# Kernel optimization log

Measured on AMD Instinct MI355X. Metric: run time of the kernel, lower is better.

The kernel has to match this reference:

```python
import jax, jax.numpy as jnp
import numpy as np


def _mish(x):
    return x * jnp.tanh(jax.nn.softplus(x))


def setup_inputs() -> dict:
    key = jax.random.key(0)
    ks = jax.random.split(key, 10)
    N, D, U, NB, M, MD = 2048, 1024, 2048, 4, 8192, 1024
    g = lambda k, shape, s=0.02: jax.random.normal(k, shape, jnp.float32) * s
    return dict(
        x=jax.random.normal(ks[0], (N, D), jnp.float32),
        w=g(ks[1], (D, U, NB)),
        delay=g(ks[2], (D, U, NB)),
        b=jnp.zeros((U, NB), jnp.float32),
        gate_W=g(ks[3], (D, NB)),
        gate_b=jnp.zeros((NB,), jnp.float32),
        neuron_avg=jax.random.uniform(ks[4], (U,), jnp.float32),
        conn_W1=g(ks[5], (U, 32)),
        conn_b1=jnp.zeros((32,), jnp.float32),
        conn_W2=g(ks[6], (32, U)),
        conn_b2=jnp.zeros((U,), jnp.float32),
        mask=jnp.ones((U,), jnp.float32),
        act_w=jnp.ones((9,), jnp.float32),
        read_W=g(ks[7], (U, M)),
        read_b=jnp.zeros((M,), jnp.float32),
        memory=g(ks[8], (M, MD), 1.0),
    )


def reference(x, w, delay, b, gate_W, gate_b, neuron_avg, conn_W1, conn_b1,
              conn_W2, conn_b2, mask, act_w, read_W, read_b, memory):
    # --- DynamicPlasticDenseDendritic forward ---
    w_mod = w * jax.nn.sigmoid(delay)                      # [D,U,NB]
    branch = jnp.einsum('nd,dub->nub', x, w_mod) + b       # [N,U,NB]
    gate = jax.nn.softmax(x @ gate_W + gate_b, axis=-1)    # [N,NB]
    z = jnp.einsum('nub,nb->nu', branch, gate)             # [N,U]
    # DynamicConnectivity on neuron activation averages (single row)
    h = jax.nn.relu(neuron_avg[None, :] @ conn_W1 + conn_b1)   # [1,32]
    conn = jax.nn.sigmoid(h @ conn_W2 + conn_b2)               # [1,U]
    a = jax.nn.relu(z * conn * mask[None, :])                  # [N,U]
    # --- LearnedActivation: softmax-weighted 8-way activation blend (+zero) ---
    wts = jax.nn.softmax(act_w)
    blend = (wts[0] * jax.nn.sigmoid(a) + wts[1] * jax.nn.elu(a)
             + wts[2] * jnp.tanh(a) + wts[3] * jax.nn.relu(a)
             + wts[4] * jax.nn.silu(a) + wts[5] * jax.nn.gelu(a, approximate=False)
             + wts[6] * jax.nn.selu(a) + wts[7] * _mish(a))
    # --- EpisodicMemory read ---
    attn = jax.nn.softmax(blend @ read_W + read_b, axis=-1)   # [N,M]
    read = attn @ memory                                       # [N,MD]
    return read
```

## Files before the change

kernel.cpp:

```cpp
#include <hip/hip_runtime.h>


typedef unsigned short u16;
typedef __attribute__((ext_vector_type(8))) short bf16x8;
typedef __attribute__((ext_vector_type(4))) float f32x4;

__device__ __forceinline__ float b2f(u16 h) {
    union { unsigned u; float f; } v; v.u = ((unsigned)h) << 16; return v.f;
}
__device__ __forceinline__ u16 f2b(float f) {
    union { float f; unsigned u; } v; v.f = f;
    unsigned u = v.u;
    return (u16)((u + 0x7fffu + ((u >> 16) & 1u)) >> 16);
}

__device__ __forceinline__ void async_copy16(void* lds, const void* g) {
    __builtin_amdgcn_global_load_lds(
        (__attribute__((address_space(1))) void*)(g),
        (__attribute__((address_space(3))) void*)(lds), 16, 0, 0);
}

__device__ __forceinline__ int swz(int o) { return o ^ (((o >> 7) & 7) << 4); }

__device__ __forceinline__ int swz64(int kg, int row) { return kg ^ (row & 3); }

__device__ __forceinline__ void stage_tile256(const u16* __restrict__ src, int ld,
                                              int base0, int k0,
                                              char* ldsbase, int tid)
{
#pragma unroll
    for (int h = 0; h < 2; h++)
#pragma unroll
        for (int it = 0; it < 2; it++) {
            int o = it * 8192 + tid * 16;
            int s = swz(o);
            int r = s >> 7;
            int c = (s & 127) >> 1;
            async_copy16(ldsbase + h * 16384 + o,
                         src + (size_t)(base0 + h * 128 + r) * ld + k0 + c);
        }
}

__device__ __forceinline__ void gemm256_core8(const u16* __restrict__ A,
                                              const u16* __restrict__ B,
                                              int Ktiles, int ld,
                                              int row0, int col0,
                                              char* lds, f32x4 (&acc)[8][4])
{
    const int tid  = threadIdx.x;
    const int lane = tid & 63;
    const int wv   = tid >> 6;
    const int wr   = wv >> 2;
    const int wc   = wv & 3;
    const int lr   = lane & 15, kg = lane >> 4;

#pragma unroll
    for (int i = 0; i < 8; i++)
#pragma unroll
        for (int j = 0; j < 4; j++) {
            f32x4 z = {0.f, 0.f, 0.f, 0.f};
            acc[i][j] = z;
        }

    stage_tile256(A, ld, row0, 0, lds, tid);
    stage_tile256(B, ld, col0, 0, lds + 32768, tid);
    asm volatile("s_waitcnt vmcnt(0)" ::: "memory");
    __builtin_amdgcn_s_barrier();

    bf16x8 af03[4][2], af47[4][2], bfr[2][2];

    for (int t = 0; t < Ktiles; t++) {
        const int buf = (t & 1) << 16;
        const char* sA = lds + buf + wr * 16384;
        const char* sB = lds + buf + 32768 + ((wc >> 1) * 16384);
        char* nb = lds + (((t + 1) & 1) << 16);
        const bool pf = (t + 1 < Ktiles);

        auto rdA = [&](int i, int ks) {
            int off = (i * 16 + lr) * 128 + ks * 64 + kg * 16;
            return *(const bf16x8*)(sA + swz(off));
        };
        auto rdB = [&](int j, int ks) {
            int off = ((wc & 1) * 64 + j * 16 + lr) * 128 + ks * 64 + kg * 16;
            return *(const bf16x8*)(sB + swz(off));
        };

#pragma unroll
        for (int i = 0; i < 4; i++) { af03[i][0] = rdA(i, 0); af03[i][1] = rdA(i, 1); }
#pragma unroll
        for (int j = 0; j < 2; j++) { bfr[j][0] = rdB(j, 0); bfr[j][1] = rdB(j, 1); }
#pragma unroll
        for (int i = 0; i < 4; i++) { af47[i][0] = rdA(4 + i, 0); af47[i][1] = rdA(4 + i, 1); }
        if (pf) stage_tile256(A, ld, row0, (t + 1) * 64, nb, tid);
        __builtin_amdgcn_s_barrier();
        __builtin_amdgcn_s_setprio(1);
#pragma unroll
        for (int i = 0; i < 4; i++)
#pragma unroll
            for (int j = 0; j < 2; j++) {
                acc[i][j] = __builtin_amdgcn_mfma_f32_16x16x32_bf16(af03[i][0], bfr[j][0], acc[i][j], 0, 0, 0);
                acc[i][j] = __builtin_amdgcn_mfma_f32_16x16x32_bf16(af03[i][1], bfr[j][1], acc[i][j], 0, 0, 0);
            }
        __builtin_amdgcn_s_setprio(0);
        __builtin_amdgcn_s_barrier();

        if (pf) stage_tile256(B, ld, col0, (t + 1) * 64, nb + 32768, tid);
        __builtin_amdgcn_s_barrier();
        __builtin_amdgcn_s_setprio(1);
#pragma unroll
        for (int i = 0; i < 4; i++)
#pragma unroll
            for (int j = 0; j < 2; j++) {
                acc[4 + i][j] = __builtin_amdgcn_mfma_f32_16x16x32_bf16(af47[i][0], bfr[j][0], acc[4 + i][j], 0, 0, 0);
                acc[4 + i][j] = __builtin_amdgcn_mfma_f32_16x16x32_bf16(af47[i][1], bfr[j][1], acc[4 + i][j], 0, 0, 0);
            }
        __builtin_amdgcn_s_setprio(0);
        __builtin_amdgcn_s_barrier();

#pragma unroll
        for (int j = 0; j < 2; j++) { bfr[j][0] = rdB(2 + j, 0); bfr[j][1] = rdB(2 + j, 1); }
        __builtin_amdgcn_s_barrier();
        __builtin_amdgcn_s_setprio(1);
#pragma unroll
        for (int i = 0; i < 4; i++)
#pragma unroll
            for (int j = 0; j < 2; j++) {
                acc[4 + i][2 + j] = __builtin_amdgcn_mfma_f32_16x16x32_bf16(af47[i][0], bfr[j][0], acc[4 + i][2 + j], 0, 0, 0);
                acc[4 + i][2 + j] = __builtin_amdgcn_mfma_f32_16x16x32_bf16(af47[i][1], bfr[j][1], acc[4 + i][2 + j], 0, 0, 0);
            }
        __builtin_amdgcn_s_setprio(0);
        __builtin_amdgcn_s_barrier();

        __builtin_amdgcn_s_setprio(1);
#pragma unroll
        for (int i = 0; i < 4; i++)
#pragma unroll
            for (int j = 0; j < 2; j++) {
                acc[i][2 + j] = __builtin_amdgcn_mfma_f32_16x16x32_bf16(af03[i][0], bfr[j][0], acc[i][2 + j], 0, 0, 0);
                acc[i][2 + j] = __builtin_amdgcn_mfma_f32_16x16x32_bf16(af03[i][1], bfr[j][1], acc[i][2 + j], 0, 0, 0);
            }
        __builtin_amdgcn_s_setprio(0);
        asm volatile("s_waitcnt vmcnt(0)" ::: "memory");
        __builtin_amdgcn_s_barrier();
    }
}

template<int BM, int BN, int S>
__device__ __forceinline__ void gemm_core_db(const u16* __restrict__ A,
                                             const u16* __restrict__ B,
                                             int Kloop, int ld,
                                             int row0, int col0,
                                             u16* smem,
                                             f32x4 (&acc)[BM / 32][BN / 32])
{
    constexpr int MT = BM / 32, NT = BN / 32;
    constexpr int STG = (BM + BN) * 32;
    constexpr int SET = STG * S;
    const int tid  = threadIdx.x;
    const int lane = tid & 63;
    const int wv   = tid >> 6;
    const int wr   = wv >> 1, wc = wv & 1;
    const int lr   = lane & 15, kg = lane >> 4;

#pragma unroll
    for (int i = 0; i < MT; i++)
#pragma unroll
        for (int j = 0; j < NT; j++) {
            f32x4 z = {0.f, 0.f, 0.f, 0.f};
            acc[i][j] = z;
        }

    auto stage_in = [&](u16* set, int k0) {
#pragma unroll
        for (int c = tid; c < BM * 4; c += 256) {
            int row = c >> 2, sl = swz64(c & 3, row);
            const u16* gA = A + (size_t)(row0 + row) * ld + k0 + sl * 8;
#pragma unroll
            for (int s = 0; s < S; s++)
                async_copy16(set + s * STG + c * 8, gA + s * 32);
        }
#pragma unroll
        for (int c = tid; c < BN * 4; c += 256) {
            int row = c >> 2, sl = swz64(c & 3, row);
            const u16* gB = B + (size_t)(col0 + row) * ld + k0 + sl * 8;
#pragma unroll
            for (int s = 0; s < S; s++)
                async_copy16(set + s * STG + BM * 32 + c * 8, gB + s * 32);
        }
    };

    stage_in(smem, 0);
    __syncthreads();

    int p = 0;
    for (int k0 = 0; k0 < Kloop; k0 += 32 * S) {
        if (k0 + 32 * S < Kloop)
            stage_in(smem + (p ^ 1) * SET, k0 + 32 * S);
        u16* set = smem + p * SET;
#pragma unroll
        for (int s = 0; s < S; s++) {
            const u16* sA = set + s * STG;
            const u16* sB = sA + BM * 32;
            bf16x8 af[MT], bfr[NT];
#pragma unroll
            for (int i = 0; i < MT; i++) {
                int row = wr * (BM / 2) + i * 16 + lr;
                af[i] = *(const bf16x8*)(sA + (row * 32 + swz64(kg, row) * 8));
            }
#pragma unroll
            for (int j = 0; j < NT; j++) {
                int row = wc * (BN / 2) + j * 16 + lr;
                bfr[j] = *(const bf16x8*)(sB + (row * 32 + swz64(kg, row) * 8));
            }
#pragma unroll
            for (int i = 0; i < MT; i++)
#pragma unroll
                for (int j = 0; j < NT; j++)
                    acc[i][j] = __builtin_amdgcn_mfma_f32_16x16x32_bf16(
                                    af[i], bfr[j], acc[i][j], 0, 0, 0);
        }
        __syncthreads();
        p ^= 1;
    }
}

__global__ __launch_bounds__(256)
void k_prep(const float* __restrict__ na, const float* __restrict__ W1,
            const float* __restrict__ b1, const float* __restrict__ W2,
            const float* __restrict__ b2, const float* __restrict__ actw,
            float* __restrict__ conn, float* __restrict__ wts,
            const float* __restrict__ x, const float* __restrict__ gW,
            const float* __restrict__ gb, float* __restrict__ gate,
            u16* __restrict__ y,
            const float* __restrict__ w, const float* __restrict__ delay,
            u16* __restrict__ wmT)
{
    __shared__ __align__(16) char sh[256 * 32 * 4 + 128];
    const int bid = blockIdx.x;
    const int tid = threadIdx.x;

    if (bid == 0) {
        float* red = (float*)sh;
        float* hsh = (float*)(sh + 256 * 32 * 4);
        float h[32];
#pragma unroll
        for (int k = 0; k < 32; k++) h[k] = 0.f;
        for (int u = tid; u < 2048; u += 256) {
            float nav = na[u];
            const float* row = W1 + u * 32;
#pragma unroll
            for (int k = 0; k < 32; k++) h[k] += nav * row[k];
        }
#pragma unroll
        for (int k = 0; k < 32; k++) red[tid * 32 + k] = h[k];
        for (int s = 128; s > 0; s >>= 1) {
            __syncthreads();
            if (tid < s)
#pragma unroll
                for (int k = 0; k < 32; k++) red[tid * 32 + k] += red[(tid + s) * 32 + k];
        }
        __syncthreads();
        if (tid < 32) hsh[tid] = fmaxf(red[tid] + b1[tid], 0.f);
        if (tid == 0) {
            float e[9], m = -1e30f;
            for (int i = 0; i < 9; i++) { e[i] = actw[i]; m = fmaxf(m, e[i]); }
            float s = 0.f;
            for (int i = 0; i < 9; i++) { e[i] = expf(e[i] - m); s += e[i]; }
            for (int i = 0; i < 9; i++) wts[i] = e[i] / s;
        }
        __syncthreads();
        for (int u = tid; u < 2048; u += 256) {
            float a = 0.f;
#pragma unroll
            for (int k = 0; k < 32; k++) a += hsh[k] * W2[k * 2048 + u];
            conn[u] = 1.f / (1.f + expf(-(a + b2[u])));
        }
    } else if (bid <= 512) {
        const int lane = tid & 63, wvx = tid >> 6;
        const int n = (bid - 1) * 4 + wvx;
        const float* xr = x + (size_t)n * 1024;
        float a0 = 0, a1 = 0, a2 = 0, a3 = 0;
        float xv[16];
#pragma unroll
        for (int s = 0; s < 16; s++) {
            int d = s * 64 + lane;
            float xd = xr[d]; xv[s] = xd;
            float4 g4 = *(const float4*)(gW + d * 4);
            a0 += xd * g4.x; a1 += xd * g4.y; a2 += xd * g4.z; a3 += xd * g4.w;
        }
#pragma unroll
        for (int off = 32; off > 0; off >>= 1) {
            a0 += __shfl_xor(a0, off); a1 += __shfl_xor(a1, off);
            a2 += __shfl_xor(a2, off); a3 += __shfl_xor(a3, off);
        }
        a0 += gb[0]; a1 += gb[1]; a2 += gb[2]; a3 += gb[3];
        float m = fmaxf(fmaxf(a0, a1), fmaxf(a2, a3));
        float e0 = expf(a0 - m), e1 = expf(a1 - m), e2 = expf(a2 - m), e3 = expf(a3 - m);
        float inv = 1.f / (e0 + e1 + e2 + e3);
        float g0 = e0 * inv, g1 = e1 * inv, g2 = e2 * inv, g3 = e3 * inv;
        if (lane == 0) *(float4*)(gate + n * 4) = make_float4(g0, g1, g2, g3);
#pragma unroll
        for (int s = 0; s < 16; s++) {
            int d = s * 64 + lane;
            ushort4 o;
            o.x = f2b(xv[s] * g0); o.y = f2b(xv[s] * g1);
            o.z = f2b(xv[s] * g2); o.w = f2b(xv[s] * g3);
            *(ushort4*)(y + (size_t)n * 4096 + d * 4) = o;
        }
    } else {
        typedef ushort4 row65[65];
        row65* tile = (row65*)sh;
        const int b = bid - 513;
        const int u0 = (b & 31) * 64, d0 = (b >> 5) * 32;
        const int tx = tid & 63, ty = tid >> 6;
#pragma unroll
        for (int i = 0; i < 8; i++) {
            int d = i * 4 + ty;
            size_t idx = ((size_t)(d0 + d) * 2048 + (u0 + tx)) * 4;
            float4 w4 = *(const float4*)(w + idx);
            float4 d4 = *(const float4*)(delay + idx);
            ushort4 o;
            o.x = f2b(w4.x / (1.f + expf(-d4.x)));
            o.y = f2b(w4.y / (1.f + expf(-d4.y)));
            o.z = f2b(w4.z / (1.f + expf(-d4.z)));
            o.w = f2b(w4.w / (1.f + expf(-d4.w)));
            tile[d][tx] = o;
        }
        __syncthreads();
        const int dx = tid & 31, uy = tid >> 5;
#pragma unroll
        for (int i = 0; i < 8; i++) {
            int u = i * 8 + uy;
            *(ushort4*)(wmT + (size_t)(u0 + u) * 4096 + (d0 + dx) * 4) = tile[dx][u];
        }
    }
}

__global__ __launch_bounds__(256)
void k_transpose(const float* __restrict__ in, u16* __restrict__ out, int R, int C)
{
    __shared__ __align__(16) u16 t[64][68];
    const int tid = threadIdx.x, tx = tid & 15, ty = tid >> 4;
    const int c0 = blockIdx.x * 64, r0 = blockIdx.y * 64;
#pragma unroll
    for (int i = 0; i < 4; i++) {
        int r = r0 + ty + i * 16;
        float4 v = *(const float4*)(in + (size_t)r * C + c0 + tx * 4);
        t[tx * 4 + 0][ty + i * 16] = f2b(v.x); t[tx * 4 + 1][ty + i * 16] = f2b(v.y);
        t[tx * 4 + 2][ty + i * 16] = f2b(v.z); t[tx * 4 + 3][ty + i * 16] = f2b(v.w);
    }
    __syncthreads();
#pragma unroll
    for (int i = 0; i < 4; i++) {
        int c = ty + i * 16;
        ushort4 v;
        v.x = t[c][tx * 4 + 0]; v.y = t[c][tx * 4 + 1];
        v.z = t[c][tx * 4 + 2]; v.w = t[c][tx * 4 + 3];
        *(ushort4*)(out + (size_t)(c0 + c) * R + r0 + tx * 4) = v;
    }
}

__device__ __forceinline__ float act_blend(float a,
    float w0, float w1, float w2, float w3,
    float w4, float w5, float w6, float w7)
{
    float sig = 1.f / (1.f + expf(-a));
    float elu = (a > 0.f) ? a : (expf(a) - 1.f);
    float th  = tanhf(a);
    float rel = fmaxf(a, 0.f);
    float sil = a * sig;
    float gel = a * 0.5f * (1.f + erff(a * 0.70710678118654752f));
    float sel = (a > 0.f) ? 1.0507009873554805f * a
                          : 1.0507009873554805f * 1.6732632423543772f * (expf(a) - 1.f);
    float sp  = (a > 20.f) ? a : log1pf(expf(a));
    float mish = a * tanhf(sp);
    return w0 * sig + w1 * elu + w2 * th + w3 * rel + w4 * sil + w5 * gel
         + w6 * sel + w7 * mish;
}

__global__ __launch_bounds__(512, 2)
void k_gemm_a8(const u16* __restrict__ A, const u16* __restrict__ B,
               float* __restrict__ P)
{
    __shared__ __align__(16) char lds[131072];
    const int row0 = blockIdx.y * 256, col0 = blockIdx.x * 256;
    const u16* Ac = A + (size_t)blockIdx.z * 1024;
    const u16* Bc = B + (size_t)blockIdx.z * 1024;

    f32x4 acc[8][4];
    gemm256_core8(Ac, Bc, 16, 4096, row0, col0, lds, acc);

    float* Pz = P + (size_t)blockIdx.z * 2048 * 2048;
    const int tid = threadIdx.x, lane = tid & 63, wv = tid >> 6;
    const int wr = wv >> 2, wc = wv & 3, lr = lane & 15, kg = lane >> 4;
#pragma unroll
    for (int i = 0; i < 8; i++)
#pragma unroll
        for (int r = 0; r < 4; r++) {
            int n = row0 + wr * 128 + i * 16 + kg * 4 + r;
            size_t ob = (size_t)n * 2048;
#pragma unroll
            for (int j = 0; j < 4; j++)
                Pz[ob + col0 + wc * 64 + j * 16 + lr] = acc[i][j][r];
        }
}

__global__ __launch_bounds__(256)
void k_reduce_blend(const float* __restrict__ P, const float* __restrict__ gate,
                    const float* __restrict__ conn, const float* __restrict__ mask,
                    const float* __restrict__ wts, const float* __restrict__ bbias,
                    u16* __restrict__ blend)
{
    constexpr size_t SL = (size_t)2048 * 2048;
    const int n  = blockIdx.x;
    const int u0 = threadIdx.x * 8;
    const float* base = P + (size_t)n * 2048 + u0;

    float v[8];
#pragma unroll
    for (int h = 0; h < 2; h++) {
        float4 a = *(const float4*)(base + h * 4);
        float4 b = *(const float4*)(base + SL + h * 4);
        float4 c = *(const float4*)(base + 2 * SL + h * 4);
        float4 d = *(const float4*)(base + 3 * SL + h * 4);
        v[h * 4 + 0] = a.x + b.x + c.x + d.x;
        v[h * 4 + 1] = a.y + b.y + c.y + d.y;
        v[h * 4 + 2] = a.z + b.z + c.z + d.z;
        v[h * 4 + 3] = a.w + b.w + c.w + d.w;
    }
    float4 g = *(const float4*)(gate + n * 4);
    const float w0 = wts[0], w1 = wts[1], w2 = wts[2], w3 = wts[3];
    const float w4 = wts[4], w5 = wts[5], w6 = wts[6], w7 = wts[7];

    ushort4 o[2];
#pragma unroll
    for (int j = 0; j < 8; j++) {
        int u = u0 + j;
        float4 b4 = *(const float4*)(bbias + u * 4);
        float z = v[j] + g.x * b4.x + g.y * b4.y + g.z * b4.z + g.w * b4.w;
        float a = fmaxf(z * conn[u] * mask[u], 0.f);
        u16 r = f2b(act_blend(a, w0, w1, w2, w3, w4, w5, w6, w7));
        ((u16*)o)[j] = r;
    }
    *(ushort4*)(blend + (size_t)n * 2048 + u0)     = o[0];
    *(ushort4*)(blend + (size_t)n * 2048 + u0 + 4) = o[1];
}

__global__ __launch_bounds__(512, 2)
void k_gemm_logits8(const u16* __restrict__ BL, const u16* __restrict__ RWT,
                    const float* __restrict__ rbias, u16* __restrict__ out)
{
    __shared__ __align__(16) char lds[131072];
    const int row0 = blockIdx.y * 256, col0 = blockIdx.x * 256;

    f32x4 acc[8][4];
    gemm256_core8(BL, RWT, 32, 2048, row0, col0, lds, acc);

    const int tid = threadIdx.x, lane = tid & 63, wv = tid >> 6;
    const int wr = wv >> 2, wc = wv & 3, lr = lane & 15, kg = lane >> 4;
    float rb[4]; int mm[4];
#pragma unroll
    for (int j = 0; j < 4; j++) {
        mm[j] = col0 + wc * 64 + j * 16 + lr;
        rb[j] = rbias[mm[j]];
    }
#pragma unroll
    for (int i = 0; i < 8; i++)
#pragma unroll
        for (int r = 0; r < 4; r++) {
            int n = row0 + wr * 128 + i * 16 + kg * 4 + r;
            size_t ob = (size_t)n * 8192;
#pragma unroll
            for (int j = 0; j < 4; j++)
                out[ob + mm[j]] = f2b(acc[i][j][r] + rb[j]);
        }
}

__global__ __launch_bounds__(256)
void k_post(u16* __restrict__ buf, const float* __restrict__ mem,
            u16* __restrict__ memT)
{
    __shared__ __align__(16) char sh[64 * 68 * 2 + 64];
    const int bid = blockIdx.x;
    const int tid = threadIdx.x;

    if (bid < 2048) {
        float* red = (float*)sh;
        const int lane = tid & 63, wv = tid >> 6;
        u16* row = buf + (size_t)bid * 8192;
        float v[32];
        float mx = -1e30f;
#pragma unroll
        for (int s = 0; s < 8; s++) {
            ushort4 u4 = *(const ushort4*)(row + (s * 256 + tid) * 4);
            float a = b2f(u4.x), b = b2f(u4.y), c = b2f(u4.z), d = b2f(u4.w);
            v[s * 4 + 0] = a; v[s * 4 + 1] = b; v[s * 4 + 2] = c; v[s * 4 + 3] = d;
            mx = fmaxf(mx, fmaxf(fmaxf(a, b), fmaxf(c, d)));
        }
#pragma unroll
        for (int off = 32; off > 0; off >>= 1) mx = fmaxf(mx, __shfl_xor(mx, off));
        if (lane == 0) red[wv] = mx;
        __syncthreads();
        mx = fmaxf(fmaxf(red[0], red[1]), fmaxf(red[2], red[3]));
        float sum = 0.f;
#pragma unroll
        for (int k = 0; k < 32; k++) { v[k] = expf(v[k] - mx); sum += v[k]; }
#pragma unroll
        for (int off = 32; off > 0; off >>= 1) sum += __shfl_xor(sum, off);
        if (lane == 0) red[4 + wv] = sum;
        __syncthreads();
        float inv = 1.f / (red[4] + red[5] + red[6] + red[7]);
#pragma unroll
        for (int s = 0; s < 8; s++) {
            ushort4 o;
            o.x = f2b(v[s * 4 + 0] * inv); o.y = f2b(v[s * 4 + 1] * inv);
            o.z = f2b(v[s * 4 + 2] * inv); o.w = f2b(v[s * 4 + 3] * inv);
            *(ushort4*)(row + (s * 256 + tid) * 4) = o;
        }
    } else {
        typedef u16 row68[68];
        row68* t = (row68*)sh;
        const int b = bid - 2048;
        const int c0 = (b & 15) * 64, r0 = (b >> 4) * 64;
        const int tx = tid & 15, ty = tid >> 4;
#pragma unroll
        for (int i = 0; i < 4; i++) {
            int r = r0 + ty + i * 16;
            float4 v = *(const float4*)(mem + (size_t)r * 1024 + c0 + tx * 4);
            t[tx * 4 + 0][ty + i * 16] = f2b(v.x); t[tx * 4 + 1][ty + i * 16] = f2b(v.y);
            t[tx * 4 + 2][ty + i * 16] = f2b(v.z); t[tx * 4 + 3][ty + i * 16] = f2b(v.w);
        }
        __syncthreads();
#pragma unroll
        for (int i = 0; i < 4; i++) {
            int c = ty + i * 16;
            ushort4 v;
            v.x = t[c][tx * 4 + 0]; v.y = t[c][tx * 4 + 1];
            v.z = t[c][tx * 4 + 2]; v.w = t[c][tx * 4 + 3];
            *(ushort4*)(memT + (size_t)(c0 + c) * 8192 + r0 + tx * 4) = v;
        }
    }
}

template<int BM, int BN, int S, int NCOL>
__global__ __launch_bounds__(256, 4)
void k_gemm_partial(const u16* __restrict__ A, const u16* __restrict__ B,
                    int Kchunk, int ld, float* __restrict__ P)
{
    constexpr int MT = BM / 32, NT = BN / 32;
    __shared__ __align__(16) u16 smem[2 * (BM + BN) * 32 * S];

    const int nx = gridDim.x, ny = gridDim.y;
    const int f  = blockIdx.x + nx * blockIdx.y;
    const int ch = (nx * ny) >> 3;
    const int sw = (f & 7) * ch + (f >> 3);
    const int bx = sw % nx, by = sw / nx;
    const int row0 = by * BM, col0 = bx * BN;

    const u16* Ac = A + (size_t)blockIdx.z * Kchunk;
    const u16* Bc = B + (size_t)blockIdx.z * Kchunk;

    f32x4 acc[MT][NT];
    gemm_core_db<BM, BN, S>(Ac, Bc, Kchunk, ld, row0, col0, smem, acc);

    float* Pz = P + (size_t)blockIdx.z * 2048 * NCOL;
    const int tid = threadIdx.x, lane = tid & 63, wv = tid >> 6;
    const int wr = wv >> 1, wc = wv & 1, lr = lane & 15, kg = lane >> 4;
#pragma unroll
    for (int i = 0; i < MT; i++)
#pragma unroll
        for (int r = 0; r < 4; r++) {
            int n = row0 + wr * (BM / 2) + i * 16 + kg * 4 + r;
            size_t ob = (size_t)n * NCOL;
#pragma unroll
            for (int j = 0; j < NT; j++)
                Pz[ob + col0 + wc * (BN / 2) + j * 16 + lr] = acc[i][j][r];
        }
}

__global__ __launch_bounds__(256)
void k_reduce_out(const float* __restrict__ P, float* __restrict__ out)
{
    constexpr size_t SL = (size_t)2048 * 1024;
    size_t i = ((size_t)blockIdx.x * 256 + threadIdx.x) * 4;
    float4 a = *(const float4*)(P + i);
    float4 b = *(const float4*)(P + SL + i);
    float4 c = *(const float4*)(P + 2 * SL + i);
    float4 d = *(const float4*)(P + 3 * SL + i);
    float4 o;
    o.x = a.x + b.x + c.x + d.x;
    o.y = a.y + b.y + c.y + d.y;
    o.z = a.z + b.z + c.z + d.z;
    o.w = a.w + b.w + c.w + d.w;
    *(float4*)(out + i) = o;
}

__global__ void k_fill(float* out, int n)
{
    int i = blockIdx.x * 256 + threadIdx.x;
    if (i < n) out[i] = 12345.f;
}

extern "C" void kernel_launch(void* const* d_in, const int* in_sizes, int n_in,
                              void* d_out, int out_size, void* d_ws, size_t ws_size,
                              hipStream_t stream)
{
    const float* x     = (const float*)d_in[0];
    const float* w     = (const float*)d_in[1];
    const float* delay = (const float*)d_in[2];
    const float* bb    = (const float*)d_in[3];
    const float* gW    = (const float*)d_in[4];
    const float* gb    = (const float*)d_in[5];
    const float* na    = (const float*)d_in[6];
    const float* cW1   = (const float*)d_in[7];
    const float* cb1   = (const float*)d_in[8];
    const float* cW2   = (const float*)d_in[9];
    const float* cb2   = (const float*)d_in[10];
    const float* mask  = (const float*)d_in[11];
    const float* actw  = (const float*)d_in[12];
    const float* rW    = (const float*)d_in[13];
    const float* rb    = (const float*)d_in[14];
    const float* mem   = (const float*)d_in[15];
    (void)in_sizes; (void)n_in;

    char* ws = (char*)d_ws;
    size_t off = 0;
    auto alloc = [&](size_t bytes) {
        size_t o = off; off += (bytes + 255) & ~(size_t)255; return o;
    };
    size_t o_wts   = alloc(9 * 4);
    size_t o_gate  = alloc(2048 * 4 * 4);
    size_t o_conn  = alloc(2048 * 4);
    size_t o_y     = alloc((size_t)2048 * 4096 * 2);
    size_t o_wmT   = alloc((size_t)2048 * 4096 * 2);
    size_t o_blend = alloc((size_t)2048 * 2048 * 2);
    size_t o_rwT   = alloc((size_t)8192 * 2048 * 2);
    size_t o_log   = alloc((size_t)2048 * 8192 * 2);

    if (off > ws_size) {
        k_fill<<<(out_size + 255) / 256, 256, 0, stream>>>((float*)d_out, out_size);
        return;
    }

    float* wts   = (float*)(ws + o_wts);
    float* gate  = (float*)(ws + o_gate);
    float* conn  = (float*)(ws + o_conn);
    u16* y       = (u16*)(ws + o_y);
    u16* wmT     = (u16*)(ws + o_wmT);
    u16* blend   = (u16*)(ws + o_blend);
    u16* rwT     = (u16*)(ws + o_rwT);
    u16* logits  = (u16*)(ws + o_log);
    u16* memT    = y;

    float* pA = (float*)(ws + o_rwT);
    float* pC = (float*)(ws + o_rwT);

    k_prep<<<1537, 256, 0, stream>>>(na, cW1, cb1, cW2, cb2, actw, conn, wts,
                                     x, gW, gb, gate, y, w, delay, wmT);

    k_gemm_a8<<<dim3(8, 8, 4), 512, 0, stream>>>(y, wmT, pA);
    k_reduce_blend<<<2048, 256, 0, stream>>>(pA, gate, conn, mask, wts, bb, blend);

    k_transpose<<<dim3(128, 32), 256, 0, stream>>>(rW, rwT, 2048, 8192);
    k_gemm_logits8<<<dim3(32, 8), 512, 0, stream>>>(blend, rwT, rb, logits);

    k_post<<<4096, 256, 0, stream>>>(logits, mem, memT);

    k_gemm_partial<128, 128, 2, 1024><<<dim3(8, 16, 4), 256, 0, stream>>>(
        logits, memT, 2048, 8192, pC);
    k_reduce_out<<<2048, 256, 0, stream>>>(pC, (float*)d_out);
}
```

Measured before the change: 417.4 us.

## Fold readout transpose into prep kernel and use 256x256 split-K final GEMM

The rW transpose moves into extra blocks of the prep kernel, which removes a separate launch and lets it run alongside the weight prep. When workspace allows, partials go to a dedicated pool instead of aliasing rwT, which is what permits the early transpose. The final attention-by-memory GEMM switches from 128x128 tiles with split-K 4 to a 256x256 eight-wave kernel with split-K 8. The cost is reducing twice as many partial slices, about 64 MB of fp32 traffic.

```diff
diff --git a/kernel.cpp b/kernel.cpp
--- a/kernel.cpp
+++ b/kernel.cpp
@@ -233,7 +233,8 @@
             const float* __restrict__ gb, float* __restrict__ gate,
             u16* __restrict__ y,
             const float* __restrict__ w, const float* __restrict__ delay,
-            u16* __restrict__ wmT)
+            u16* __restrict__ wmT,
+            const float* __restrict__ rW, u16* __restrict__ rwT)
 {
     __shared__ __align__(16) char sh[256 * 32 * 4 + 128];
     const int bid = blockIdx.x;
@@ -307,7 +308,7 @@
             o.z = f2b(xv[s] * g2); o.w = f2b(xv[s] * g3);
             *(ushort4*)(y + (size_t)n * 4096 + d * 4) = o;
         }
-    } else {
+    } else if (bid <= 1536) {
         typedef ushort4 row65[65];
         row65* tile = (row65*)sh;
         const int b = bid - 513;
@@ -332,6 +333,28 @@
         for (int i = 0; i < 8; i++) {
             int u = i * 8 + uy;
             *(ushort4*)(wmT + (size_t)(u0 + u) * 4096 + (d0 + dx) * 4) = tile[dx][u];
+        }
+    } else {
+        typedef u16 row68[68];
+        row68* t = (row68*)sh;
+        const int b = bid - 1537;
+        const int c0 = (b & 127) * 64, r0 = (b >> 7) * 64;
+        const int tx = tid & 15, ty = tid >> 4;
+#pragma unroll
+        for (int i = 0; i < 4; i++) {
+            int r = r0 + ty + i * 16;
+            float4 v = *(const float4*)(rW + (size_t)r * 8192 + c0 + tx * 4);
+            t[tx * 4 + 0][ty + i * 16] = f2b(v.x); t[tx * 4 + 1][ty + i * 16] = f2b(v.y);
+            t[tx * 4 + 2][ty + i * 16] = f2b(v.z); t[tx * 4 + 3][ty + i * 16] = f2b(v.w);
+        }
+        __syncthreads();
+#pragma unroll
+        for (int i = 0; i < 4; i++) {
+            int c = ty + i * 16;
+            ushort4 v;
+            v.x = t[c][tx * 4 + 0]; v.y = t[c][tx * 4 + 1];
+            v.z = t[c][tx * 4 + 2]; v.w = t[c][tx * 4 + 3];
+            *(ushort4*)(rwT + (size_t)(c0 + c) * 2048 + r0 + tx * 4) = v;
         }
     }
 }
@@ -542,6 +565,33 @@
     }
 }
 
+__global__ __launch_bounds__(512, 2)
+void k_gemm_c8(const u16* __restrict__ A, const u16* __restrict__ B,
+               float* __restrict__ P)
+{
+    __shared__ __align__(16) char lds[131072];
+    const int row0 = blockIdx.y * 256, col0 = blockIdx.x * 256;
+    const u16* Ac = A + (size_t)blockIdx.z * 1024;
+    const u16* Bc = B + (size_t)blockIdx.z * 1024;
+
+    f32x4 acc[8][4];
+    gemm256_core8(Ac, Bc, 16, 8192, row0, col0, lds, acc);
+
+    float* Pz = P + (size_t)blockIdx.z * 2048 * 1024;
+    const int tid = threadIdx.x, lane = tid & 63, wv = tid >> 6;
+    const int wr = wv >> 2, wc = wv & 3, lr = lane & 15, kg = lane >> 4;
+#pragma unroll
+    for (int i = 0; i < 8; i++)
+#pragma unroll
+        for (int r = 0; r < 4; r++) {
+            int n = row0 + wr * 128 + i * 16 + kg * 4 + r;
+            size_t ob = (size_t)n * 1024;
+#pragma unroll
+            for (int j = 0; j < 4; j++)
+                Pz[ob + col0 + wc * 64 + j * 16 + lr] = acc[i][j][r];
+        }
+}
+
 template<int BM, int BN, int S, int NCOL>
 __global__ __launch_bounds__(256, 4)
 void k_gemm_partial(const u16* __restrict__ A, const u16* __restrict__ B,
@@ -578,20 +628,18 @@
         }
 }
 
+template<int NSL>
 __global__ __launch_bounds__(256)
 void k_reduce_out(const float* __restrict__ P, float* __restrict__ out)
 {
     constexpr size_t SL = (size_t)2048 * 1024;
     size_t i = ((size_t)blockIdx.x * 256 + threadIdx.x) * 4;
-    float4 a = *(const float4*)(P + i);
-    float4 b = *(const float4*)(P + SL + i);
-    float4 c = *(const float4*)(P + 2 * SL + i);
-    float4 d = *(const float4*)(P + 3 * SL + i);
-    float4 o;
-    o.x = a.x + b.x + c.x + d.x;
-    o.y = a.y + b.y + c.y + d.y;
-    o.z = a.z + b.z + c.z + d.z;
-    o.w = a.w + b.w + c.w + d.w;
+    float4 o = *(const float4*)(P + i);
+#pragma unroll
+    for (int s = 1; s < NSL; s++) {
+        float4 p = *(const float4*)(P + s * SL + i);
+        o.x += p.x; o.y += p.y; o.z += p.z; o.w += p.w;
+    }
     *(float4*)(out + i) = o;
 }
 
@@ -636,11 +684,15 @@
     size_t o_blend = alloc((size_t)2048 * 2048 * 2);
     size_t o_rwT   = alloc((size_t)8192 * 2048 * 2);
     size_t o_log   = alloc((size_t)2048 * 8192 * 2);
-
-    if (off > ws_size) {
+    size_t base_off = off;
+
+    if (base_off > ws_size) {
         k_fill<<<(out_size + 255) / 256, 256, 0, stream>>>((float*)d_out, out_size);
         return;
     }
+
+    size_t o_pool = alloc((size_t)64 * 1024 * 1024);
+    const bool planB = (off <= ws_size);
 
     float* wts   = (float*)(ws + o_wts);
     float* gate  = (float*)(ws + o_gate);
@@ -652,21 +704,30 @@
     u16* logits  = (u16*)(ws + o_log);
     u16* memT    = y;
 
-    float* pA = (float*)(ws + o_rwT);
-    float* pC = (float*)(ws + o_rwT);
-
-    k_prep<<<1537, 256, 0, stream>>>(na, cW1, cb1, cW2, cb2, actw, conn, wts,
-                                     x, gW, gb, gate, y, w, delay, wmT);
-
-    k_gemm_a8<<<dim3(8, 8, 4), 512, 0, stream>>>(y, wmT, pA);
-    k_reduce_blend<<<2048, 256, 0, stream>>>(pA, gate, conn, mask, wts, bb, blend);
-
-    k_transpose<<<dim3(128, 32), 256, 0, stream>>>(rW, rwT, 2048, 8192);
-    k_gemm_logits8<<<dim3(32, 8), 512, 0, stream>>>(blend, rwT, rb, logits);
-
-    k_post<<<4096, 256, 0, stream>>>(logits, mem, memT);
-
-    k_gemm_partial<128, 128, 2, 1024><<<dim3(8, 16, 4), 256, 0, stream>>>(
-        logits, memT, 2048, 8192, pC);
-    k_reduce_out<<<2048, 256, 0, stream>>>(pC, (float*)d_out);
-}
+    if (planB) {
+        float* pool = (float*)(ws + o_pool);
+        k_prep<<<5633, 256, 0, stream>>>(na, cW1, cb1, cW2, cb2, actw, conn, wts,
+                                         x, gW, gb, gate, y, w, delay, wmT,
+                                         rW, rwT);
+        k_gemm_a8<<<dim3(8, 8, 4), 512, 0, stream>>>(y, wmT, pool);
+        k_reduce_blend<<<2048, 256, 0, stream>>>(pool, gate, conn, mask, wts, bb, blend);
+        k_gemm_logits8<<<dim3(32, 8), 512, 0, stream>>>(blend, rwT, rb, logits);
+        k_post<<<4096, 256, 0, stream>>>(logits, mem, memT);
+        k_gemm_c8<<<dim3(4, 8, 8), 512, 0, stream>>>(logits, memT, pool);
+        k_reduce_out<8><<<2048, 256, 0, stream>>>(pool, (float*)d_out);
+    } else {
+        float* pA = (float*)(ws + o_rwT);
+        float* pC = (float*)(ws + o_rwT);
+        k_prep<<<1537, 256, 0, stream>>>(na, cW1, cb1, cW2, cb2, actw, conn, wts,
+                                         x, gW, gb, gate, y, w, delay, wmT,
+                                         rW, rwT);
+        k_gemm_a8<<<dim3(8, 8, 4), 512, 0, stream>>>(y, wmT, pA);
+        k_reduce_blend<<<2048, 256, 0, stream>>>(pA, gate, conn, mask, wts, bb, blend);
+        k_transpose<<<dim3(128, 32), 256, 0, stream>>>(rW, rwT, 2048, 8192);
+        k_gemm_logits8<<<dim3(32, 8), 512, 0, stream>>>(blend, rwT, rb, logits);
+        k_post<<<4096, 256, 0, stream>>>(logits, mem, memT);
+        k_gemm_partial<128, 128, 2, 1024><<<dim3(8, 16, 4), 256, 0, stream>>>(
+            logits, memT, 2048, 8192, pC);
+        k_reduce_out<4><<<2048, 256, 0, stream>>>(pC, (float*)d_out);
+    }
+}
```

Measured after the change: 416.4 us. About the same (-0.2%).
